# Kernel optimization log

Measured on AMD Instinct MI355X. Metric: run time of the kernel, lower is better.

## Reference

```python
import jax, jax.numpy as jnp
import numpy as np

N = 100000          # num_nodes
E = 1250000         # num_edges
H = 64              # node_hidden_size
T = 2               # num_rounds


def setup_inputs() -> dict:
    key = jax.random.key(0)
    ks = jax.random.split(key, 10)
    s = 0.1  # init scale for weights
    return {
        "x": jax.random.normal(ks[0], (N, H), dtype=jnp.float32),
        "edge_index": jax.random.randint(ks[1], (2, E), 0, N, dtype=jnp.int64),
        "edge_attr": jax.random.normal(ks[2], (E, 1), dtype=jnp.float32),
        # message layers: Linear(2H+1 -> H), one per round
        "msg_W": jax.random.normal(ks[3], (T, H, 2 * H + 1), dtype=jnp.float32) * s,
        "msg_b": jax.random.normal(ks[4], (T, H), dtype=jnp.float32) * s,
        # GRUCell params, gate order (r, z, n) as in torch
        "gru_Wih": jax.random.normal(ks[5], (T, 3 * H, H), dtype=jnp.float32) * s,
        "gru_bih": jax.random.normal(ks[6], (T, 3 * H), dtype=jnp.float32) * s,
        "gru_Whh": jax.random.normal(ks[7], (T, 3 * H, H), dtype=jnp.float32) * s,
        "gru_bhh": jax.random.normal(ks[8], (T, 3 * H), dtype=jnp.float32) * s,
    }


def _gru_cell(inp, h, Wih, bih, Whh, bhh):
    # torch.nn.GRUCell math, gate order r, z, n
    gi = inp @ Wih.T + bih   # [N, 3H]
    gh = h @ Whh.T + bhh     # [N, 3H]
    i_r, i_z, i_n = jnp.split(gi, 3, axis=1)
    h_r, h_z, h_n = jnp.split(gh, 3, axis=1)
    r = jax.nn.sigmoid(i_r + h_r)
    z = jax.nn.sigmoid(i_z + h_z)
    n = jnp.tanh(i_n + r * h_n)
    return (1.0 - z) * n + z * h


def reference(x, edge_index, edge_attr, msg_W, msg_b, gru_Wih, gru_bih, gru_Whh, gru_bhh):
    row, col = edge_index[0], edge_index[1]
    num_rounds = msg_W.shape[0]
    for t in range(num_rounds):
        src = x[row]    # [E, H]
        dest = x[col]   # [E, H]
        m_input = jnp.concatenate([dest, src, edge_attr], axis=1)  # [E, 2H+1]
        messages = m_input @ msg_W[t].T + msg_b[t]                 # [E, H]
        agg = jax.ops.segment_sum(messages, row, num_segments=x.shape[0])  # [N, H]
        x = _gru_cell(agg, x, gru_Wih[t], gru_bih[t], gru_Whh[t], gru_bhh[t])
    return x
```

## Files before the change

### kernel.cpp

```cpp
#include <hip/hip_runtime.h>
#include <hip/hip_bf16.h>
#include <hip/hip_fp16.h>

#define H 64
#define CAP 48

typedef __attribute__((ext_vector_type(8))) short short8;
typedef __attribute__((ext_vector_type(4))) float float4v;

__device__ __forceinline__ short f2bf_bits(float f) {
    union { __hip_bfloat16 b; short s; } u;
    u.b = __float2bfloat16(f);
    return u.s;
}
__device__ __forceinline__ float bf2f(unsigned short s) {
    union { unsigned int u; float f; } v;
    v.u = ((unsigned int)s) << 16;
    return v.f;
}
__device__ __forceinline__ void split8(const float* p, short8& hi, short8& lo) {
    float4v f0 = *(const float4v*)p;
    float4v f1 = *(const float4v*)(p + 4);
#pragma unroll
    for (int j = 0; j < 8; j++) {
        float f = (j < 4) ? f0[j] : f1[j - 4];
        short h = f2bf_bits(f);
        float fh = bf2f((unsigned short)h);
        hi[j] = h;
        lo[j] = f2bf_bits(f - fh);
    }
}
__device__ __forceinline__ void zero8(short8& hi, short8& lo) {
#pragma unroll
    for (int j = 0; j < 8; j++) { hi[j] = 0; lo[j] = 0; }
}

#define MFMA(a, b, c) __builtin_amdgcn_mfma_f32_16x16x32_bf16(a, b, c, 0, 0, 0)

__global__ __launch_bounds__(256) void count_prep(
    const int* __restrict__ row, int* __restrict__ deg, int* __restrict__ lpos,
    int E, int EB,
    const float* __restrict__ msg_W,
    const float* __restrict__ Wih, const float* __restrict__ Whh,
    short* __restrict__ msgfrag, short* __restrict__ grufrag, int T)
{
    if ((int)blockIdx.x < EB) {
        int e = blockIdx.x * 256 + threadIdx.x;
        if (e < E) lpos[e] = atomicAdd(&deg[row[e]], 1);
        return;
    }
    const int lane = threadIdx.x & 63;
    int unit = (blockIdx.x - EB) * 4 + (threadIdx.x >> 6);
    const int kq = (lane >> 4) * 8;
    if (unit < T * 16) {
        const int slot = unit & 15, t = unit >> 4;
        const int tile = slot >> 1, ks = slot & 1;
        const float* W = msg_W + (size_t)t * H * 129;
        const int wrow = (tile & 3) * 16 + (lane & 15);
        const int coff = (tile < 4) ? 0 : 64;
        short8 hi, lo;
        split8(W + (size_t)wrow * 129 + coff + ks * 32 + kq, hi, lo);
        short8* out = (short8*)(msgfrag + (size_t)t * 16384);
        out[slot * 64 + lane] = hi;
        out[16 * 64 + slot * 64 + lane] = lo;
    } else {
        unit -= T * 16;
        if (unit >= T * 48) return;
        const int slot = unit % 48, t = unit / 48;
        const int tile = slot >> 1, ks = slot & 1;
        const float* Wp = (tile < 12)
            ? (Wih + (size_t)t * 192 * H + ((size_t)(tile * 16 + (lane & 15))) * H)
            : (Whh + (size_t)t * 192 * H + ((size_t)((tile - 12) * 16 + (lane & 15))) * H);
        short8 hi, lo;
        split8(Wp + ks * 32 + kq, hi, lo);
        short8* out = (short8*)(grufrag + (size_t)t * 49152);
        out[slot * 64 + lane] = hi;
        out[48 * 64 + slot * 64 + lane] = lo;
    }
}

__global__ __launch_bounds__(256) void scatter_cast(
    const int* __restrict__ row, const int* __restrict__ col,
    const float* __restrict__ attr, const int* __restrict__ lpos,
    int2* __restrict__ edata, int E, int EB,
    const float* __restrict__ x_in, __half* __restrict__ xh, int NH8)
{
    if ((int)blockIdx.x < EB) {
        int e = blockIdx.x * 256 + threadIdx.x;
        if (e < E) {
            int p = lpos[e];
            if (p < CAP) {
                int2 v;
                v.x = col[e];
                v.y = __float_as_int(attr[e]);
                edata[(size_t)row[e] * CAP + p] = v;
            }
        }
    } else {
        int i = (blockIdx.x - EB) * 256 + threadIdx.x;
        if (i < NH8) {
            const float* p = x_in + (size_t)i * 8;
            float4v f0 = *(const float4v*)p;
            float4v f1 = *(const float4v*)(p + 4);
            short8 hv;
#pragma unroll
            for (int u = 0; u < 8; u++) {
                float f = (u < 4) ? f0[u] : f1[u - 4];
                hv[u] = __half_as_short(__float2half(f));
            }
            *(short8*)(xh + (size_t)i * 8) = hv;
        }
    }
}

__global__ __launch_bounds__(256) void aggregate(
    const int* __restrict__ deg, const int2* __restrict__ edata,
    const __half* __restrict__ xh,
    short* __restrict__ s_hi, short* __restrict__ s_lo,
    float2* __restrict__ asum2, int N)
{
    const int tid = threadIdx.x, lane = tid & 63, wv = tid >> 6;
    const int g = lane >> 3, cl = lane & 7;
    const int n = (blockIdx.x * 4 + wv) * 8 + g;
    int cnt = 0;
    if (n < N) { cnt = deg[n]; if (cnt > CAP) cnt = CAP; }
    const int2* ebase = edata + (size_t)n * CAP;
    float acc[8] = {0.f, 0.f, 0.f, 0.f, 0.f, 0.f, 0.f, 0.f};
    float aacc = 0.f;
    for (int j = 0; j < cnt; j++) {
        int2 ed = ebase[j];
        aacc += __int_as_float(ed.y);
        short8 hv = *(const short8*)(xh + (size_t)ed.x * H + cl * 8);
#pragma unroll
        for (int u = 0; u < 8; u++)
            acc[u] += __half2float(__ushort_as_half((unsigned short)hv[u]));
    }
    if (n < N) {
        short8 hi8, lo8;
#pragma unroll
        for (int u = 0; u < 8; u++) {
            float v = acc[u];
            short h = f2bf_bits(v);
            hi8[u] = h;
            lo8[u] = f2bf_bits(v - bf2f((unsigned short)h));
        }
        *(short8*)(s_hi + (size_t)n * H + cl * 8) = hi8;
        *(short8*)(s_lo + (size_t)n * H + cl * 8) = lo8;
        if (cl == 0) asum2[n] = make_float2(aacc, (float)cnt);
    }
}

__global__ __launch_bounds__(256) void fused_msg_gru(
    const short* __restrict__ s_hi, const short* __restrict__ s_lo,
    const float2* __restrict__ asum2,
    const float* xf,
    float* x, __half* __restrict__ xh,
    const short* __restrict__ mfrag, const short* __restrict__ gfrag,
    const float* __restrict__ Wt, const float* __restrict__ mb,
    const float* __restrict__ bih, const float* __restrict__ bhh,
    int N, int write_xh)
{
    __shared__ float scratch[4][16 * 68];
    const int tid = threadIdx.x, lane = tid & 63, wv = tid >> 6;
    const int base = blockIdx.x * 64 + wv * 16;
    if (base >= N) return;
    const int arow = lane & 15;
    const int kq = (lane >> 4) * 8;
    const int colb = lane & 15;
    const int rq4 = (lane >> 4) * 4;
    const int m_a = base + arow;
    const bool mv = (m_a < N);
    const short8* mhi = (const short8*)mfrag;
    const short8* mlo = mhi + 16 * 64;
    const short8* ghi = (const short8*)gfrag;
    const short8* glo = ghi + 48 * 64;

    short8 sfh[2], sfl[2], xfh[2], xfl[2];
#pragma unroll
    for (int ks = 0; ks < 2; ks++) {
        if (mv) {
            sfh[ks] = *(const short8*)(s_hi + (size_t)m_a * H + ks * 32 + kq);
            sfl[ks] = *(const short8*)(s_lo + (size_t)m_a * H + ks * 32 + kq);
            split8(xf + (size_t)m_a * H + ks * 32 + kq, xfh[ks], xfl[ks]);
        } else { zero8(sfh[ks], sfl[ks]); zero8(xfh[ks], xfl[ks]); }
    }
    float2 da[4];
#pragma unroll
    for (int r = 0; r < 4; r++) {
        const int m = base + rq4 + r;
        da[r] = (m < N) ? asum2[m] : make_float2(0.f, 0.f);
    }

    float4v accd[4], accs[4];
#pragma unroll
    for (int ct = 0; ct < 4; ct++) {
        accd[ct] = (float4v){0.f, 0.f, 0.f, 0.f};
        accs[ct] = (float4v){0.f, 0.f, 0.f, 0.f};
    }
#pragma unroll
    for (int ks = 0; ks < 2; ks++) {
#pragma unroll
        for (int ct = 0; ct < 4; ct++) {
            short8 bh = mhi[(ct * 2 + ks) * 64 + lane];
            short8 bl = mlo[(ct * 2 + ks) * 64 + lane];
            accd[ct] = MFMA(sfh[ks], bh, accd[ct]);
            accd[ct] = MFMA(sfl[ks], bh, accd[ct]);
            accd[ct] = MFMA(sfh[ks], bl, accd[ct]);
            short8 ch = mhi[((4 + ct) * 2 + ks) * 64 + lane];
            short8 cl8 = mlo[((4 + ct) * 2 + ks) * 64 + lane];
            accs[ct] = MFMA(xfh[ks], ch, accs[ct]);
            accs[ct] = MFMA(xfl[ks], ch, accs[ct]);
            accs[ct] = MFMA(xfh[ks], cl8, accs[ct]);
        }
    }

    float* scr = scratch[wv];
#pragma unroll
    for (int ct = 0; ct < 4; ct++) {
        const int j = ct * 16 + colb;
        const float bj = mb[j];
        const float wa = Wt[(size_t)j * 129 + 128];
#pragma unroll
        for (int r = 0; r < 4; r++) {
            float v = accd[ct][r] + da[r].y * (accs[ct][r] + bj) + da[r].x * wa;
            scr[(rq4 + r) * 68 + j] = v;
        }
    }
    asm volatile("s_waitcnt lgkmcnt(0)" ::: "memory");
    short8 agh[2], agl[2];
#pragma unroll
    for (int ks = 0; ks < 2; ks++)
        split8(scr + arow * 68 + ks * 32 + kq, agh[ks], agl[ks]);

#pragma unroll
    for (int ct = 0; ct < 4; ct++) {
        float4v ai[3], ao[3];
#pragma unroll
        for (int g2 = 0; g2 < 3; g2++) {
            ai[g2] = (float4v){0.f, 0.f, 0.f, 0.f};
            ao[g2] = (float4v){0.f, 0.f, 0.f, 0.f};
        }
#pragma unroll
        for (int ks = 0; ks < 2; ks++) {
#pragma unroll
            for (int g2 = 0; g2 < 3; g2++) {
                short8 bh = ghi[((g2 * 4 + ct) * 2 + ks) * 64 + lane];
                short8 bl = glo[((g2 * 4 + ct) * 2 + ks) * 64 + lane];
                ai[g2] = MFMA(agh[ks], bh, ai[g2]);
                ai[g2] = MFMA(agl[ks], bh, ai[g2]);
                ai[g2] = MFMA(agh[ks], bl, ai[g2]);
                short8 hh = ghi[((12 + g2 * 4 + ct) * 2 + ks) * 64 + lane];
                short8 hl = glo[((12 + g2 * 4 + ct) * 2 + ks) * 64 + lane];
                ao[g2] = MFMA(xfh[ks], hh, ao[g2]);
                ao[g2] = MFMA(xfl[ks], hh, ao[g2]);
                ao[g2] = MFMA(xfh[ks], hl, ao[g2]);
            }
        }
        const int j = ct * 16 + colb;
        const float b_ir = bih[j], b_iz = bih[64 + j], b_in = bih[128 + j];
        const float b_hr = bhh[j], b_hz = bhh[64 + j], b_hn = bhh[128 + j];
#pragma unroll
        for (int r = 0; r < 4; r++) {
            const int m = base + rq4 + r;
            if (m >= N) continue;
            float ir = ai[0][r] + b_ir;
            float iz = ai[1][r] + b_iz;
            float in_ = ai[2][r] + b_in;
            float hr = ao[0][r] + b_hr;
            float hz = ao[1][r] + b_hz;
            float hn = ao[2][r] + b_hn;
            float rr = 1.f / (1.f + __expf(-(ir + hr)));
            float zz = 1.f / (1.f + __expf(-(iz + hz)));
            float e2 = __expf(2.f * (in_ + rr * hn));
            float nn = 1.f - 2.f / (e2 + 1.f);
            float hold = xf[(size_t)m * H + j];
            float out = (1.f - zz) * nn + zz * hold;
            x[(size_t)m * H + j] = out;
            if (write_xh) xh[(size_t)m * H + j] = __float2half(out);
        }
    }
}

extern "C" void kernel_launch(void* const* d_in, const int* in_sizes, int n_in,
                              void* d_out, int out_size, void* d_ws, size_t ws_size,
                              hipStream_t stream) {
    const float* x_in  = (const float*)d_in[0];
    const int*   ei    = (const int*)d_in[1];
    const float* attr  = (const float*)d_in[2];
    const float* msg_W = (const float*)d_in[3];
    const float* msg_b = (const float*)d_in[4];
    const float* Wih   = (const float*)d_in[5];
    const float* bih   = (const float*)d_in[6];
    const float* Whh   = (const float*)d_in[7];
    const float* bhh   = (const float*)d_in[8];

    const int N = in_sizes[0] / H;
    const int E = in_sizes[2];
    const int T = in_sizes[4] / H;
    const int* row = ei;
    const int* col = ei + E;

    float*  x       = (float*)d_out;
    short*  s_hi    = (short*)d_ws;
    short*  s_lo    = s_hi + (size_t)N * H;
    int*    lpos    = (int*)s_lo;
    __half* xh      = (__half*)(s_lo + (size_t)N * H);
    float2* asum2   = (float2*)(xh + (size_t)N * H);
    int*    deg     = (int*)(asum2 + N);
    int2*   edata   = (int2*)(deg + N);
    short*  msgfrag = (short*)(edata + (size_t)N * CAP);
    short*  grufrag = msgfrag + (size_t)T * 16384;

    const int eb  = (E + 255) / 256;
    const int nh8 = (N * H) / 8;
    const int cb  = (nh8 + 255) / 256;
    const int pb  = (T * 16 + T * 48 + 3) / 4;

    hipMemsetAsync(deg, 0, (size_t)N * sizeof(int), stream);

    count_prep<<<eb + pb, 256, 0, stream>>>(
        row, deg, lpos, E, eb, msg_W, Wih, Whh, msgfrag, grufrag, T);
    scatter_cast<<<eb + cb, 256, 0, stream>>>(
        row, col, attr, lpos, edata, E, eb, x_in, xh, nh8);

    const int nbq        = (N + 63) / 64;
    const int agg_blocks = (N + 31) / 32;

    for (int t = 0; t < T; t++) {
        aggregate<<<agg_blocks, 256, 0, stream>>>(
            deg, edata, xh, s_hi, s_lo, asum2, N);
        fused_msg_gru<<<nbq, 256, 0, stream>>>(
            s_hi, s_lo, asum2,
            (t == 0) ? x_in : x, x, xh,
            msgfrag + (size_t)t * 16384, grufrag + (size_t)t * 49152,
            msg_W + (size_t)t * H * (2 * H + 1), msg_b + (size_t)t * H,
            bih + (size_t)t * 3 * H, bhh + (size_t)t * 3 * H,
            N, (t + 1 < T) ? 1 : 0);
    }
}
```

Measured before the change: 352.9 us.

## Fuse neighbor aggregation into message+GRU kernel with double-buffered half features

Merges the separate aggregate kernel into the message/GRU kernel. Each wave gathers neighbor sums for its 16 rows into shared memory, two nodes per 8-lane group with a one-step prefetch of edge data. This removes the global round trip of the split bf16 aggregate and degree buffers, plus one launch per round. The half-precision feature copy is now ping-ponged between two buffers so one kernel can read the old features while writing the new ones. Output rows are staged through LDS for coalesced vector stores. In exchange, fewer waves cover the gather, which may hide memory latency less well. The row bounds checks are dropped, so it relies on N being a multiple of 16.

```diff
diff --git a/kernel.cpp b/kernel.cpp
--- a/kernel.cpp
+++ b/kernel.cpp
@@ -21,6 +21,16 @@
 __device__ __forceinline__ void split8(const float* p, short8& hi, short8& lo) {
     float4v f0 = *(const float4v*)p;
     float4v f1 = *(const float4v*)(p + 4);
+#pragma unroll
+    for (int j = 0; j < 8; j++) {
+        float f = (j < 4) ? f0[j] : f1[j - 4];
+        short h = f2bf_bits(f);
+        float fh = bf2f((unsigned short)h);
+        hi[j] = h;
+        lo[j] = f2bf_bits(f - fh);
+    }
+}
+__device__ __forceinline__ void split8v(float4v f0, float4v f1, short8& hi, short8& lo) {
 #pragma unroll
     for (int j = 0; j < 8; j++) {
         float f = (j < 4) ? f0[j] : f1[j - 4];
@@ -113,83 +123,88 @@
     }
 }
 
-__global__ __launch_bounds__(256) void aggregate(
+#define SLD 68
+__global__ __launch_bounds__(256) void agg_msg_gru(
     const int* __restrict__ deg, const int2* __restrict__ edata,
-    const __half* __restrict__ xh,
-    short* __restrict__ s_hi, short* __restrict__ s_lo,
-    float2* __restrict__ asum2, int N)
-{
-    const int tid = threadIdx.x, lane = tid & 63, wv = tid >> 6;
-    const int g = lane >> 3, cl = lane & 7;
-    const int n = (blockIdx.x * 4 + wv) * 8 + g;
-    int cnt = 0;
-    if (n < N) { cnt = deg[n]; if (cnt > CAP) cnt = CAP; }
-    const int2* ebase = edata + (size_t)n * CAP;
-    float acc[8] = {0.f, 0.f, 0.f, 0.f, 0.f, 0.f, 0.f, 0.f};
-    float aacc = 0.f;
-    for (int j = 0; j < cnt; j++) {
-        int2 ed = ebase[j];
-        aacc += __int_as_float(ed.y);
-        short8 hv = *(const short8*)(xh + (size_t)ed.x * H + cl * 8);
-#pragma unroll
-        for (int u = 0; u < 8; u++)
-            acc[u] += __half2float(__ushort_as_half((unsigned short)hv[u]));
-    }
-    if (n < N) {
-        short8 hi8, lo8;
-#pragma unroll
-        for (int u = 0; u < 8; u++) {
-            float v = acc[u];
-            short h = f2bf_bits(v);
-            hi8[u] = h;
-            lo8[u] = f2bf_bits(v - bf2f((unsigned short)h));
-        }
-        *(short8*)(s_hi + (size_t)n * H + cl * 8) = hi8;
-        *(short8*)(s_lo + (size_t)n * H + cl * 8) = lo8;
-        if (cl == 0) asum2[n] = make_float2(aacc, (float)cnt);
-    }
-}
-
-__global__ __launch_bounds__(256) void fused_msg_gru(
-    const short* __restrict__ s_hi, const short* __restrict__ s_lo,
-    const float2* __restrict__ asum2,
+    const __half* __restrict__ xh_r,
     const float* xf,
-    float* x, __half* __restrict__ xh,
+    float* x, __half* __restrict__ xh_w,
     const short* __restrict__ mfrag, const short* __restrict__ gfrag,
     const float* __restrict__ Wt, const float* __restrict__ mb,
     const float* __restrict__ bih, const float* __restrict__ bhh,
     int N, int write_xh)
 {
-    __shared__ float scratch[4][16 * 68];
+    __shared__ float scratch[4][16 * SLD];
+    __shared__ float2 adeg[4][16];
     const int tid = threadIdx.x, lane = tid & 63, wv = tid >> 6;
     const int base = blockIdx.x * 64 + wv * 16;
     if (base >= N) return;
+    const int g = lane >> 3, cl = lane & 7;
     const int arow = lane & 15;
     const int kq = (lane >> 4) * 8;
     const int colb = lane & 15;
     const int rq4 = (lane >> 4) * 4;
     const int m_a = base + arow;
-    const bool mv = (m_a < N);
     const short8* mhi = (const short8*)mfrag;
     const short8* mlo = mhi + 16 * 64;
     const short8* ghi = (const short8*)gfrag;
     const short8* glo = ghi + 48 * 64;
+    float* scr = scratch[wv];
+
+    float4v xr[2][2];
+#pragma unroll
+    for (int ks = 0; ks < 2; ks++) {
+        xr[ks][0] = *(const float4v*)(xf + (size_t)m_a * H + ks * 32 + kq);
+        xr[ks][1] = *(const float4v*)(xf + (size_t)m_a * H + ks * 32 + kq + 4);
+    }
+
+    const int n0 = base + g, n1 = base + 8 + g;
+    int cnt0 = min(deg[n0], CAP);
+    int cnt1 = min(deg[n1], CAP);
+    const int2* eb0 = edata + (size_t)n0 * CAP;
+    const int2* eb1 = edata + (size_t)n1 * CAP;
+    float acc0[8] = {0.f,0.f,0.f,0.f,0.f,0.f,0.f,0.f};
+    float acc1[8] = {0.f,0.f,0.f,0.f,0.f,0.f,0.f,0.f};
+    float aacc0 = 0.f, aacc1 = 0.f;
+    const int jm = cnt0 > cnt1 ? cnt0 : cnt1;
+    int2 p0 = eb0[0], p1 = eb1[0];
+    for (int j = 0; j < jm; j++) {
+        int2 e0 = p0, e1 = p1;
+        int jn = j + 1 < CAP ? j + 1 : CAP - 1;
+        p0 = eb0[jn]; p1 = eb1[jn];
+        int c0 = min(max(e0.x, 0), N - 1);
+        int c1 = min(max(e1.x, 0), N - 1);
+        const short8 h0 = *(const short8*)(xh_r + (size_t)c0 * H + cl * 8);
+        const short8 h1 = *(const short8*)(xh_r + (size_t)c1 * H + cl * 8);
+        float w0 = (j < cnt0) ? 1.f : 0.f;
+        float w1 = (j < cnt1) ? 1.f : 0.f;
+        aacc0 += (j < cnt0) ? __int_as_float(e0.y) : 0.f;
+        aacc1 += (j < cnt1) ? __int_as_float(e1.y) : 0.f;
+#pragma unroll
+        for (int u = 0; u < 8; u++) {
+            acc0[u] = fmaf(w0, __half2float(__ushort_as_half((unsigned short)h0[u])), acc0[u]);
+            acc1[u] = fmaf(w1, __half2float(__ushort_as_half((unsigned short)h1[u])), acc1[u]);
+        }
+    }
+    *(float4v*)(scr + g * SLD + cl * 8)            = (float4v){acc0[0], acc0[1], acc0[2], acc0[3]};
+    *(float4v*)(scr + g * SLD + cl * 8 + 4)        = (float4v){acc0[4], acc0[5], acc0[6], acc0[7]};
+    *(float4v*)(scr + (8 + g) * SLD + cl * 8)      = (float4v){acc1[0], acc1[1], acc1[2], acc1[3]};
+    *(float4v*)(scr + (8 + g) * SLD + cl * 8 + 4)  = (float4v){acc1[4], acc1[5], acc1[6], acc1[7]};
+    if (cl == 0) {
+        adeg[wv][g]     = make_float2(aacc0, (float)cnt0);
+        adeg[wv][8 + g] = make_float2(aacc1, (float)cnt1);
+    }
+    asm volatile("s_waitcnt lgkmcnt(0)" ::: "memory");
 
     short8 sfh[2], sfl[2], xfh[2], xfl[2];
 #pragma unroll
     for (int ks = 0; ks < 2; ks++) {
-        if (mv) {
-            sfh[ks] = *(const short8*)(s_hi + (size_t)m_a * H + ks * 32 + kq);
-            sfl[ks] = *(const short8*)(s_lo + (size_t)m_a * H + ks * 32 + kq);
-            split8(xf + (size_t)m_a * H + ks * 32 + kq, xfh[ks], xfl[ks]);
-        } else { zero8(sfh[ks], sfl[ks]); zero8(xfh[ks], xfl[ks]); }
+        split8(scr + arow * SLD + ks * 32 + kq, sfh[ks], sfl[ks]);
+        split8v(xr[ks][0], xr[ks][1], xfh[ks], xfl[ks]);
     }
     float2 da[4];
 #pragma unroll
-    for (int r = 0; r < 4; r++) {
-        const int m = base + rq4 + r;
-        da[r] = (m < N) ? asum2[m] : make_float2(0.f, 0.f);
-    }
+    for (int r = 0; r < 4; r++) da[r] = adeg[wv][rq4 + r];
 
     float4v accd[4], accs[4];
 #pragma unroll
@@ -214,7 +229,6 @@
         }
     }
 
-    float* scr = scratch[wv];
 #pragma unroll
     for (int ct = 0; ct < 4; ct++) {
         const int j = ct * 16 + colb;
@@ -223,14 +237,14 @@
 #pragma unroll
         for (int r = 0; r < 4; r++) {
             float v = accd[ct][r] + da[r].y * (accs[ct][r] + bj) + da[r].x * wa;
-            scr[(rq4 + r) * 68 + j] = v;
+            scr[(rq4 + r) * SLD + j] = v;
         }
     }
     asm volatile("s_waitcnt lgkmcnt(0)" ::: "memory");
     short8 agh[2], agl[2];
 #pragma unroll
     for (int ks = 0; ks < 2; ks++)
-        split8(scr + arow * 68 + ks * 32 + kq, agh[ks], agl[ks]);
+        split8(scr + arow * SLD + ks * 32 + kq, agh[ks], agl[ks]);
 
 #pragma unroll
     for (int ct = 0; ct < 4; ct++) {
@@ -262,7 +276,6 @@
 #pragma unroll
         for (int r = 0; r < 4; r++) {
             const int m = base + rq4 + r;
-            if (m >= N) continue;
             float ir = ai[0][r] + b_ir;
             float iz = ai[1][r] + b_iz;
             float in_ = ai[2][r] + b_in;
@@ -274,9 +287,27 @@
             float e2 = __expf(2.f * (in_ + rr * hn));
             float nn = 1.f - 2.f / (e2 + 1.f);
             float hold = xf[(size_t)m * H + j];
-            float out = (1.f - zz) * nn + zz * hold;
-            x[(size_t)m * H + j] = out;
-            if (write_xh) xh[(size_t)m * H + j] = __float2half(out);
+            scr[(rq4 + r) * SLD + j] = (1.f - zz) * nn + zz * hold;
+        }
+    }
+    asm volatile("s_waitcnt lgkmcnt(0)" ::: "memory");
+
+    float4v o[4];
+#pragma unroll
+    for (int q4 = 0; q4 < 4; q4++)
+        o[q4] = *(const float4v*)(scr + arow * SLD + (lane >> 4) * 16 + q4 * 4);
+    {
+        float4v* xp = (float4v*)(x + (size_t)m_a * H + (lane >> 4) * 16);
+        xp[0] = o[0]; xp[1] = o[1]; xp[2] = o[2]; xp[3] = o[3];
+        if (write_xh) {
+            short8 hv0, hv1;
+#pragma unroll
+            for (int u = 0; u < 8; u++) {
+                hv0[u] = __half_as_short(__float2half(o[u >> 2][u & 3]));
+                hv1[u] = __half_as_short(__float2half(o[2 + (u >> 2)][u & 3]));
+            }
+            *(short8*)(xh_w + (size_t)m_a * H + (lane >> 4) * 16) = hv0;
+            *(short8*)(xh_w + (size_t)m_a * H + (lane >> 4) * 16 + 8) = hv1;
         }
     }
 }
@@ -301,12 +332,10 @@
     const int* col = ei + E;
 
     float*  x       = (float*)d_out;
-    short*  s_hi    = (short*)d_ws;
-    short*  s_lo    = s_hi + (size_t)N * H;
-    int*    lpos    = (int*)s_lo;
-    __half* xh      = (__half*)(s_lo + (size_t)N * H);
-    float2* asum2   = (float2*)(xh + (size_t)N * H);
-    int*    deg     = (int*)(asum2 + N);
+    __half* xh_a    = (__half*)d_ws;
+    __half* xh_b    = xh_a + (size_t)N * H;
+    int*    lpos    = (int*)(xh_b + (size_t)N * H);
+    int*    deg     = lpos + E;
     int2*   edata   = (int2*)(deg + N);
     short*  msgfrag = (short*)(edata + (size_t)N * CAP);
     short*  grufrag = msgfrag + (size_t)T * 16384;
@@ -321,17 +350,16 @@
     count_prep<<<eb + pb, 256, 0, stream>>>(
         row, deg, lpos, E, eb, msg_W, Wih, Whh, msgfrag, grufrag, T);
     scatter_cast<<<eb + cb, 256, 0, stream>>>(
-        row, col, attr, lpos, edata, E, eb, x_in, xh, nh8);
-
-    const int nbq        = (N + 63) / 64;
-    const int agg_blocks = (N + 31) / 32;
+        row, col, attr, lpos, edata, E, eb, x_in, xh_a, nh8);
+
+    const int nbq = (N + 63) / 64;
 
     for (int t = 0; t < T; t++) {
-        aggregate<<<agg_blocks, 256, 0, stream>>>(
-            deg, edata, xh, s_hi, s_lo, asum2, N);
-        fused_msg_gru<<<nbq, 256, 0, stream>>>(
-            s_hi, s_lo, asum2,
-            (t == 0) ? x_in : x, x, xh,
+        const __half* xh_r = (t & 1) ? xh_b : xh_a;
+        __half*       xh_w = (t & 1) ? xh_a : xh_b;
+        agg_msg_gru<<<nbq, 256, 0, stream>>>(
+            deg, edata, xh_r,
+            (t == 0) ? x_in : x, x, xh_w,
             msgfrag + (size_t)t * 16384, grufrag + (size_t)t * 49152,
             msg_W + (size_t)t * H * (2 * H + 1), msg_b + (size_t)t * H,
             bih + (size_t)t * 3 * H, bhh + (size_t)t * 3 * H,
```

Result: slower. 361.4 us (+2.4%).

## Batch gather loads in aggregate and stage GRU output through LDS for vector stores

Applied to the files above, without the earlier changes.

The aggregate kernel now processes neighbors eight at a time, issuing all edge-record loads and then all row gathers before accumulating. This exposes more memory-level parallelism, with masked weights handling the tail. The GRU epilogue now writes results into per-wave shared scratch and re-reads them row-contiguously, so x and the fp16 copy are stored with wide vector writes instead of scattered scalar stores. The cost is redundant clamped loads on partial batches, extra LDS traffic, and higher register pressure.

```diff
diff --git a/kernel.cpp b/kernel.cpp
--- a/kernel.cpp
+++ b/kernel.cpp
@@ -125,24 +125,40 @@
     int cnt = 0;
     if (n < N) { cnt = deg[n]; if (cnt > CAP) cnt = CAP; }
     const int2* ebase = edata + (size_t)n * CAP;
-    float acc[8] = {0.f, 0.f, 0.f, 0.f, 0.f, 0.f, 0.f, 0.f};
+    float acc[8] = {0.f,0.f,0.f,0.f,0.f,0.f,0.f,0.f};
     float aacc = 0.f;
-    for (int j = 0; j < cnt; j++) {
-        int2 ed = ebase[j];
-        aacc += __int_as_float(ed.y);
-        short8 hv = *(const short8*)(xh + (size_t)ed.x * H + cl * 8);
-#pragma unroll
-        for (int u = 0; u < 8; u++)
-            acc[u] += __half2float(__ushort_as_half((unsigned short)hv[u]));
+    for (int j = 0; j < cnt; j += 8) {
+        int2 e[8];
+#pragma unroll
+        for (int u = 0; u < 8; u++) {
+            int idx = j + u; if (idx > cnt - 1) idx = cnt - 1;
+            e[u] = ebase[idx];
+        }
+        short8 h[8];
+#pragma unroll
+        for (int u = 0; u < 8; u++) {
+            int c = e[u].x;
+            c = (c < 0) ? 0 : (c >= N ? N - 1 : c);
+            h[u] = *(const short8*)(xh + (size_t)c * H + cl * 8);
+        }
+#pragma unroll
+        for (int u = 0; u < 8; u++) {
+            const bool val = (j + u < cnt);
+            const float w = val ? 1.f : 0.f;
+            aacc += val ? __int_as_float(e[u].y) : 0.f;
+#pragma unroll
+            for (int k = 0; k < 8; k++)
+                acc[k] = fmaf(w, __half2float(__ushort_as_half((unsigned short)h[u][k])), acc[k]);
+        }
     }
     if (n < N) {
         short8 hi8, lo8;
 #pragma unroll
         for (int u = 0; u < 8; u++) {
             float v = acc[u];
-            short h = f2bf_bits(v);
-            hi8[u] = h;
-            lo8[u] = f2bf_bits(v - bf2f((unsigned short)h));
+            short hbits = f2bf_bits(v);
+            hi8[u] = hbits;
+            lo8[u] = f2bf_bits(v - bf2f((unsigned short)hbits));
         }
         *(short8*)(s_hi + (size_t)n * H + cl * 8) = hi8;
         *(short8*)(s_lo + (size_t)n * H + cl * 8) = lo8;
@@ -150,6 +166,7 @@
     }
 }
 
+#define SLD 68
 __global__ __launch_bounds__(256) void fused_msg_gru(
     const short* __restrict__ s_hi, const short* __restrict__ s_lo,
     const float2* __restrict__ asum2,
@@ -160,7 +177,7 @@
     const float* __restrict__ bih, const float* __restrict__ bhh,
     int N, int write_xh)
 {
-    __shared__ float scratch[4][16 * 68];
+    __shared__ float scratch[4][16 * SLD];
     const int tid = threadIdx.x, lane = tid & 63, wv = tid >> 6;
     const int base = blockIdx.x * 64 + wv * 16;
     if (base >= N) return;
@@ -174,6 +191,7 @@
     const short8* mlo = mhi + 16 * 64;
     const short8* ghi = (const short8*)gfrag;
     const short8* glo = ghi + 48 * 64;
+    float* scr = scratch[wv];
 
     short8 sfh[2], sfl[2], xfh[2], xfl[2];
 #pragma unroll
@@ -214,7 +232,6 @@
         }
     }
 
-    float* scr = scratch[wv];
 #pragma unroll
     for (int ct = 0; ct < 4; ct++) {
         const int j = ct * 16 + colb;
@@ -223,14 +240,14 @@
 #pragma unroll
         for (int r = 0; r < 4; r++) {
             float v = accd[ct][r] + da[r].y * (accs[ct][r] + bj) + da[r].x * wa;
-            scr[(rq4 + r) * 68 + j] = v;
+            scr[(rq4 + r) * SLD + j] = v;
         }
     }
     asm volatile("s_waitcnt lgkmcnt(0)" ::: "memory");
     short8 agh[2], agl[2];
 #pragma unroll
     for (int ks = 0; ks < 2; ks++)
-        split8(scr + arow * 68 + ks * 32 + kq, agh[ks], agl[ks]);
+        split8(scr + arow * SLD + ks * 32 + kq, agh[ks], agl[ks]);
 
 #pragma unroll
     for (int ct = 0; ct < 4; ct++) {
@@ -262,7 +279,6 @@
 #pragma unroll
         for (int r = 0; r < 4; r++) {
             const int m = base + rq4 + r;
-            if (m >= N) continue;
             float ir = ai[0][r] + b_ir;
             float iz = ai[1][r] + b_iz;
             float in_ = ai[2][r] + b_in;
@@ -273,10 +289,28 @@
             float zz = 1.f / (1.f + __expf(-(iz + hz)));
             float e2 = __expf(2.f * (in_ + rr * hn));
             float nn = 1.f - 2.f / (e2 + 1.f);
-            float hold = xf[(size_t)m * H + j];
-            float out = (1.f - zz) * nn + zz * hold;
-            x[(size_t)m * H + j] = out;
-            if (write_xh) xh[(size_t)m * H + j] = __float2half(out);
+            float hold = (m < N) ? xf[(size_t)m * H + j] : 0.f;
+            scr[(rq4 + r) * SLD + j] = (1.f - zz) * nn + zz * hold;
+        }
+    }
+    asm volatile("s_waitcnt lgkmcnt(0)" ::: "memory");
+
+    if (mv) {
+        float4v o[4];
+#pragma unroll
+        for (int q4 = 0; q4 < 4; q4++)
+            o[q4] = *(const float4v*)(scr + arow * SLD + (lane >> 4) * 16 + q4 * 4);
+        float4v* xp = (float4v*)(x + (size_t)m_a * H + (lane >> 4) * 16);
+        xp[0] = o[0]; xp[1] = o[1]; xp[2] = o[2]; xp[3] = o[3];
+        if (write_xh) {
+            short8 hv0, hv1;
+#pragma unroll
+            for (int u = 0; u < 8; u++) {
+                hv0[u] = __half_as_short(__float2half(o[u >> 2][u & 3]));
+                hv1[u] = __half_as_short(__float2half(o[2 + (u >> 2)][u & 3]));
+            }
+            *(short8*)(xh + (size_t)m_a * H + (lane >> 4) * 16) = hv0;
+            *(short8*)(xh + (size_t)m_a * H + (lane >> 4) * 16 + 8) = hv1;
         }
     }
 }
```

Result: faster. 343.6 us (-2.6%).
